# Optimization experiments

Hardware: AMD Instinct MI355X
Metric: run time of the kernel (lower is better)

The kernel has to match this reference:

```python
import jax, jax.numpy as jnp
import numpy as np
import math

D_MODEL = 96
D_STATE = 16
IMG = 32
KSZ = 3
V_LIST = [(0, 0), (0, 1), (0, -1), (1, 0), (-1, 0)]
NUM_V = len(V_LIST)
GROUPS = 4
BATCH = 4


def group_norm(x, gamma, beta, groups=GROUPS, eps=1e-5):
    B, C, H, W = x.shape
    xg = x.reshape(B, groups, C // groups, H, W)
    mu = xg.mean(axis=(2, 3, 4), keepdims=True)
    var = xg.var(axis=(2, 3, 4), keepdims=True)
    xn = ((xg - mu) * jax.lax.rsqrt(var + eps)).reshape(B, C, H, W)
    return xn * gamma[None, :, None, None] + beta[None, :, None, None]


def circ_conv(x, w, b=None):
    # circular padding then VALID conv == padding_mode='circular'
    p = w.shape[-1] // 2
    xp = jnp.pad(x, ((0, 0), (0, 0), (p, p), (p, p)), mode='wrap')
    y = jax.lax.conv_general_dilated(xp, w, (1, 1), 'VALID',
                                     dimension_numbers=('NCHW', 'OIHW', 'NCHW'))
    if b is not None:
        y = y + b[None, :, None, None]
    return y


def setup_inputs() -> dict:
    key = jax.random.key(0)
    ks = jax.random.split(key, 8)
    fan = D_MODEL * KSZ * KSZ
    inp = {
        'u_t': jax.random.normal(ks[0], (BATCH, D_MODEL, IMG, IMG), jnp.float32),
        's_prev': jax.random.normal(ks[1], (BATCH, NUM_V, D_MODEL, D_STATE, IMG, IMG), jnp.float32) * 0.1,
        'gamma': jnp.ones((D_MODEL,), jnp.float32),
        'beta': jnp.zeros((D_MODEL,), jnp.float32),
        'w_delta': jax.random.normal(ks[2], (D_MODEL, D_MODEL, KSZ, KSZ), jnp.float32) / np.sqrt(fan),
        'b_delta': jnp.zeros((D_MODEL,), jnp.float32),
        'w_B': jax.random.normal(ks[3], (D_STATE, D_MODEL, KSZ, KSZ), jnp.float32) / np.sqrt(fan),
        'w_C': jax.random.normal(ks[4], (D_STATE, D_MODEL, KSZ, KSZ), jnp.float32) / np.sqrt(fan),
        'log_A_real': jnp.full((D_MODEL, D_STATE), math.log(0.5), jnp.float32),
        'D_param': jnp.ones((D_MODEL,), jnp.float32),
        'dt_inv_softplus': jnp.asarray(math.log(math.exp(1.0) - 1.0), jnp.float32),
    }
    return inp


def reference(u_t, s_prev, gamma, beta, w_delta, b_delta, w_B, w_C, log_A_real, D_param, dt_inv_softplus):
    B, D, H, W = u_t.shape
    N = D_STATE
    u_norm = group_norm(u_t, gamma, beta)
    delta = jax.nn.softplus(circ_conv(u_norm, w_delta, b_delta) + dt_inv_softplus)
    delta = jnp.clip(delta, 1e-4, 5.0)                          # (B,D,H,W)
    B_val = circ_conv(u_norm, w_B)                               # (B,N,H,W)
    C_val = circ_conv(u_norm, w_C)                               # (B,N,H,W)
    A = -jnp.exp(log_A_real)                                     # (D,N)
    delta_bc = delta[:, :, None]                                 # (B,D,1,H,W)
    A_bar = jnp.exp(delta_bc * A[None, :, :, None, None])        # (B,D,N,H,W)
    B_bar = delta_bc * B_val[:, None]                            # (B,D,N,H,W)
    # flow transport: dest[y,x] = src[(y-vy)%H,(x-vx)%W] == roll by (vy,vx)
    s_tr = jnp.stack([jnp.roll(s_prev[:, i], shift=v, axis=(-2, -1))
                      for i, v in enumerate(V_LIST)], axis=1)    # (B,V,D,N,H,W)
    s_new = A_bar[:, None] * s_tr + B_bar[:, None] * u_t[:, None, :, None]
    y_state = jnp.sum(s_new * C_val[:, None, None], axis=3)      # (B,V,D,H,W)
    y_out = y_state + u_t[:, None] * D_param[None, None, :, None, None]
    return (y_out, s_new)
```

## Files before the change

### kernel.cpp

```cpp
#include <hip/hip_runtime.h>
#include <math.h>

#define D_MODEL 96
#define D_STATE 16
#define IMG 32
#define NUM_V 5
#define GROUPS 4
#define BATCH 4
#define HW (IMG*IMG)
#define CPG (D_MODEL/GROUPS)
#define NCOEF (D_MODEL + 2*D_STATE)
#define Y_SIZE (BATCH*NUM_V*D_MODEL*HW)

typedef float f32x4 __attribute__((ext_vector_type(4)));

__device__ __forceinline__ void nt_store4(const float4& v, float4* p) {
    f32x4 tmp = {v.x, v.y, v.z, v.w};
    __builtin_nontemporal_store(tmp, (f32x4*)p);
}

__global__ __launch_bounds__(256) void gn_kernel(const float4* __restrict__ u4,
                                                 const float* __restrict__ gamma,
                                                 const float* __restrict__ beta,
                                                 float4* __restrict__ unorm4) {
    int b = blockIdx.x >> 2, g = blockIdx.x & 3;
    int t = threadIdx.x;
    const int base4 = ((b * D_MODEL + g * CPG) * HW) >> 2;
    const int n4 = (CPG * HW) >> 2;
    float s = 0.f, s2 = 0.f;
    for (int k = t; k < n4; k += 256) {
        float4 v = u4[base4 + k];
        s += v.x + v.y + v.z + v.w;
        s2 = fmaf(v.x, v.x, fmaf(v.y, v.y, fmaf(v.z, v.z, fmaf(v.w, v.w, s2))));
    }
    for (int off = 32; off; off >>= 1) {
        s  += __shfl_down(s,  off);
        s2 += __shfl_down(s2, off);
    }
    __shared__ float red[8];
    int wid = t >> 6;
    if ((t & 63) == 0) { red[wid * 2] = s; red[wid * 2 + 1] = s2; }
    __syncthreads();
    if (t == 0) {
        float S = 0.f, S2 = 0.f;
        for (int i = 0; i < 4; ++i) { S += red[i * 2]; S2 += red[i * 2 + 1]; }
        float nf = (float)(CPG * HW);
        float mu  = S / nf;
        float var = S2 / nf - mu * mu;
        red[0] = mu;
        red[1] = rsqrtf(var + 1e-5f);
    }
    __syncthreads();
    float mu = red[0], rs = red[1];
    for (int k = t; k < n4; k += 256) {
        int c = g * CPG + (k >> 8);
        float ga = gamma[c] * rs, be = beta[c] - mu * gamma[c] * rs;
        float4 v = u4[base4 + k];
        float4 o;
        o.x = fmaf(v.x, ga, be); o.y = fmaf(v.y, ga, be);
        o.z = fmaf(v.z, ga, be); o.w = fmaf(v.w, ga, be);
        unorm4[base4 + k] = o;
    }
}

__global__ __launch_bounds__(256) void conv_kernel(const float4* __restrict__ unorm4,
                                                   const float* __restrict__ w_delta,
                                                   const float* __restrict__ b_delta,
                                                   const float* __restrict__ w_B,
                                                   const float* __restrict__ w_C,
                                                   const float* __restrict__ dt_ptr,
                                                   float4* __restrict__ coef4) {
    int bid = blockIdx.x;
    int b  = bid >> 7;
    int oc = bid & 127;
    int t  = threadIdx.x;
    int h  = t >> 3;
    int j  = t & 7;
    int lane = t & 63;
    int ll = (lane & 56) | ((j + 7) & 7);
    int rl = (lane & 56) | ((j + 1) & 7);

    const float* wp;
    float bias;
    bool is_delta = false;
    if (oc < D_MODEL) {
        wp = w_delta + oc * D_MODEL * 9;
        bias = b_delta[oc] + dt_ptr[0];
        is_delta = true;
    } else if (oc < D_MODEL + D_STATE) {
        wp = w_B + (oc - D_MODEL) * D_MODEL * 9;
        bias = 0.f;
    } else {
        wp = w_C + (oc - D_MODEL - D_STATE) * D_MODEL * 9;
        bias = 0.f;
    }
    const float4* ub4 = unorm4 + ((b * D_MODEL * HW) >> 2);

    float4 acc = {bias, bias, bias, bias};
    int hm = (h + 31) & 31, hp = (h + 1) & 31;
    int ro[3] = {hm * 8 + j, h * 8 + j, hp * 8 + j};

    for (int ic = 0; ic < D_MODEL; ++ic) {
        const float* wr = wp + ic * 9;
        const int icb = ic * 256;
        #pragma unroll
        for (int kh = 0; kh < 3; ++kh) {
            float4 q = ub4[icb + ro[kh]];
            float lw = __shfl(q.w, ll);
            float rx = __shfl(q.x, rl);
            float wa = wr[kh * 3 + 0], wb = wr[kh * 3 + 1], wc = wr[kh * 3 + 2];
            acc.x = fmaf(wa, lw,  fmaf(wb, q.x, fmaf(wc, q.y, acc.x)));
            acc.y = fmaf(wa, q.x, fmaf(wb, q.y, fmaf(wc, q.z, acc.y)));
            acc.z = fmaf(wa, q.y, fmaf(wb, q.z, fmaf(wc, q.w, acc.z)));
            acc.w = fmaf(wa, q.z, fmaf(wb, q.w, fmaf(wc, rx,  acc.w)));
        }
    }
    if (is_delta) {
        float* a = (float*)&acc;
        #pragma unroll
        for (int k = 0; k < 4; ++k) {
            float x = a[k];
            float sp = x > 20.f ? x : log1pf(__expf(x));
            a[k] = fminf(fmaxf(sp, 1e-4f), 5.f);
        }
    }
    coef4[((b * NCOEF + oc) * HW >> 2) + h * 8 + j] = acc;
}

__global__ __launch_bounds__(128) void state_kernel(const float4* __restrict__ u4,
                                                    const float4* __restrict__ s_prev4,
                                                    const float4* __restrict__ coef4,
                                                    const float* __restrict__ log_A,
                                                    const float* __restrict__ D_param,
                                                    float4* __restrict__ out4) {
    int bid = blockIdx.x;
    int b = bid / 192;
    int r = bid - b * 192;
    int d = r >> 1;
    int half = r & 1;
    int t = threadIdx.x;
    int h = half * 16 + (t >> 3);
    int j = t & 7;
    int lane = t & 63;
    int ll = (lane & 56) | ((j + 7) & 7);
    int rl = (lane & 56) | ((j + 1) & 7);
    int hw4 = h * 8 + j;

    float4 delta = coef4[((b * NCOEF + d) * HW >> 2) + hw4];
    float4 u     = u4[((b * D_MODEL + d) * HW >> 2) + hw4];
    float Dp     = D_param[d];
    const float* lA = log_A + d * D_STATE;

    int pb[NUM_V];
    #pragma unroll
    for (int i = 0; i < NUM_V; ++i)
        pb[i] = ((b * NUM_V + i) * D_MODEL + d) * (D_STATE * HW / 4);
    int hm4 = (((h + 31) & 31) * 8) + j;
    int hp4 = (((h + 1) & 31) * 8) + j;

    float4* outs4 = out4 + (Y_SIZE >> 2);

    float4 y0 = {0,0,0,0}, y1 = {0,0,0,0}, y2 = {0,0,0,0}, y3 = {0,0,0,0}, y4v = {0,0,0,0};

    #pragma unroll 2
    for (int n = 0; n < D_STATE; ++n) {
        int n4 = n * (HW / 4);
        float4 Bv = coef4[((b * NCOEF + D_MODEL + n) * HW >> 2) + hw4];
        float4 Cv = coef4[((b * NCOEF + D_MODEL + D_STATE + n) * HW >> 2) + hw4];
        float A = -__expf(lA[n]);
        float4 Ab, bu;
        Ab.x = __expf(delta.x * A); Ab.y = __expf(delta.y * A);
        Ab.z = __expf(delta.z * A); Ab.w = __expf(delta.w * A);
        bu.x = delta.x * Bv.x * u.x; bu.y = delta.y * Bv.y * u.y;
        bu.z = delta.z * Bv.z * u.z; bu.w = delta.w * Bv.w * u.w;

        {
            float4 s = s_prev4[pb[0] + n4 + hw4];
            float4 sn;
            sn.x = fmaf(Ab.x, s.x, bu.x); sn.y = fmaf(Ab.y, s.y, bu.y);
            sn.z = fmaf(Ab.z, s.z, bu.z); sn.w = fmaf(Ab.w, s.w, bu.w);
            nt_store4(sn, &outs4[pb[0] + n4 + hw4]);
            y0.x = fmaf(sn.x, Cv.x, y0.x); y0.y = fmaf(sn.y, Cv.y, y0.y);
            y0.z = fmaf(sn.z, Cv.z, y0.z); y0.w = fmaf(sn.w, Cv.w, y0.w);
        }
        {
            float4 q = s_prev4[pb[1] + n4 + hw4];
            float lw = __shfl(q.w, ll);
            float4 s = {lw, q.x, q.y, q.z};
            float4 sn;
            sn.x = fmaf(Ab.x, s.x, bu.x); sn.y = fmaf(Ab.y, s.y, bu.y);
            sn.z = fmaf(Ab.z, s.z, bu.z); sn.w = fmaf(Ab.w, s.w, bu.w);
            nt_store4(sn, &outs4[pb[1] + n4 + hw4]);
            y1.x = fmaf(sn.x, Cv.x, y1.x); y1.y = fmaf(sn.y, Cv.y, y1.y);
            y1.z = fmaf(sn.z, Cv.z, y1.z); y1.w = fmaf(sn.w, Cv.w, y1.w);
        }
        {
            float4 q = s_prev4[pb[2] + n4 + hw4];
            float rx = __shfl(q.x, rl);
            float4 s = {q.y, q.z, q.w, rx};
            float4 sn;
            sn.x = fmaf(Ab.x, s.x, bu.x); sn.y = fmaf(Ab.y, s.y, bu.y);
            sn.z = fmaf(Ab.z, s.z, bu.z); sn.w = fmaf(Ab.w, s.w, bu.w);
            nt_store4(sn, &outs4[pb[2] + n4 + hw4]);
            y2.x = fmaf(sn.x, Cv.x, y2.x); y2.y = fmaf(sn.y, Cv.y, y2.y);
            y2.z = fmaf(sn.z, Cv.z, y2.z); y2.w = fmaf(sn.w, Cv.w, y2.w);
        }
        {
            float4 s = s_prev4[pb[3] + n4 + hm4];
            float4 sn;
            sn.x = fmaf(Ab.x, s.x, bu.x); sn.y = fmaf(Ab.y, s.y, bu.y);
            sn.z = fmaf(Ab.z, s.z, bu.z); sn.w = fmaf(Ab.w, s.w, bu.w);
            nt_store4(sn, &outs4[pb[3] + n4 + hw4]);
            y3.x = fmaf(sn.x, Cv.x, y3.x); y3.y = fmaf(sn.y, Cv.y, y3.y);
            y3.z = fmaf(sn.z, Cv.z, y3.z); y3.w = fmaf(sn.w, Cv.w, y3.w);
        }
        {
            float4 s = s_prev4[pb[4] + n4 + hp4];
            float4 sn;
            sn.x = fmaf(Ab.x, s.x, bu.x); sn.y = fmaf(Ab.y, s.y, bu.y);
            sn.z = fmaf(Ab.z, s.z, bu.z); sn.w = fmaf(Ab.w, s.w, bu.w);
            nt_store4(sn, &outs4[pb[4] + n4 + hw4]);
            y4v.x = fmaf(sn.x, Cv.x, y4v.x); y4v.y = fmaf(sn.y, Cv.y, y4v.y);
            y4v.z = fmaf(sn.z, Cv.z, y4v.z); y4v.w = fmaf(sn.w, Cv.w, y4v.w);
        }
    }

    float4 du;
    du.x = u.x * Dp; du.y = u.y * Dp; du.z = u.z * Dp; du.w = u.w * Dp;
    float4* yy[NUM_V] = {&y0, &y1, &y2, &y3, &y4v};
    #pragma unroll
    for (int i = 0; i < NUM_V; ++i) {
        float4 o;
        o.x = yy[i]->x + du.x; o.y = yy[i]->y + du.y;
        o.z = yy[i]->z + du.z; o.w = yy[i]->w + du.w;
        out4[(((b * NUM_V + i) * D_MODEL + d) * HW >> 2) + hw4] = o;
    }
}

extern "C" void kernel_launch(void* const* d_in, const int* in_sizes, int n_in,
                              void* d_out, int out_size, void* d_ws, size_t ws_size,
                              hipStream_t stream) {
    const float* u_t     = (const float*)d_in[0];
    const float* s_prev  = (const float*)d_in[1];
    const float* gamma   = (const float*)d_in[2];
    const float* beta    = (const float*)d_in[3];
    const float* w_delta = (const float*)d_in[4];
    const float* b_delta = (const float*)d_in[5];
    const float* w_B     = (const float*)d_in[6];
    const float* w_C     = (const float*)d_in[7];
    const float* log_A   = (const float*)d_in[8];
    const float* D_param = (const float*)d_in[9];
    const float* dt_ptr  = (const float*)d_in[10];
    float* out = (float*)d_out;

    float* unorm = (float*)d_ws;
    float* coef  = unorm + BATCH * D_MODEL * HW;

    hipLaunchKernelGGL(gn_kernel, dim3(BATCH * GROUPS), dim3(256), 0, stream,
                       (const float4*)u_t, gamma, beta, (float4*)unorm);
    hipLaunchKernelGGL(conv_kernel, dim3(BATCH * NCOEF), dim3(256), 0, stream,
                       (const float4*)unorm, w_delta, b_delta, w_B, w_C, dt_ptr,
                       (float4*)coef);
    hipLaunchKernelGGL(state_kernel, dim3(768), dim3(128), 0, stream,
                       (const float4*)u_t, (const float4*)s_prev, (const float4*)coef,
                       log_A, D_param, (float4*)out);
}
```

Baseline: 310.2 us.

## Split state kernel across directions: one block per (batch, direction, channel)

The state kernel now launches one 256-thread block per (batch, direction, channel), each covering a full 32x32 image, instead of 128-thread blocks that each handled half an image for all five directions. Each thread processes a single direction, so it keeps one accumulator and issues one s_prev load per state step, which cuts register pressure and gives many more blocks to fill the GPU. The cost is that A_bar, B*u*delta, B and C are now recomputed and reloaded five times, once per direction.

```diff
diff --git a/kernel.cpp b/kernel.cpp
--- a/kernel.cpp
+++ b/kernel.cpp
@@ -127,46 +127,50 @@
     coef4[((b * NCOEF + oc) * HW >> 2) + h * 8 + j] = acc;
 }
 
-__global__ __launch_bounds__(128) void state_kernel(const float4* __restrict__ u4,
+__global__ __launch_bounds__(256) void state_kernel(const float4* __restrict__ u4,
                                                     const float4* __restrict__ s_prev4,
                                                     const float4* __restrict__ coef4,
                                                     const float* __restrict__ log_A,
                                                     const float* __restrict__ D_param,
                                                     float4* __restrict__ out4) {
     int bid = blockIdx.x;
-    int b = bid / 192;
-    int r = bid - b * 192;
-    int d = r >> 1;
-    int half = r & 1;
+    int b = bid / (NUM_V * D_MODEL);
+    int r = bid - b * (NUM_V * D_MODEL);
+    int i = r / D_MODEL;
+    int d = r - i * D_MODEL;
+
     int t = threadIdx.x;
-    int h = half * 16 + (t >> 3);
+    int h = t >> 3;
     int j = t & 7;
     int lane = t & 63;
     int ll = (lane & 56) | ((j + 7) & 7);
     int rl = (lane & 56) | ((j + 1) & 7);
-    int hw4 = h * 8 + j;
+    int hw4 = t;
+
+    int src4 = hw4;
+    if (i == 3) src4 = (((h + 31) & 31) << 3) | j;
+    if (i == 4) src4 = (((h + 1) & 31) << 3) | j;
+    const int mode = (i == 1) ? 1 : (i == 2) ? 2 : 0;
 
     float4 delta = coef4[((b * NCOEF + d) * HW >> 2) + hw4];
     float4 u     = u4[((b * D_MODEL + d) * HW >> 2) + hw4];
     float Dp     = D_param[d];
     const float* lA = log_A + d * D_STATE;
 
-    int pb[NUM_V];
-    #pragma unroll
-    for (int i = 0; i < NUM_V; ++i)
-        pb[i] = ((b * NUM_V + i) * D_MODEL + d) * (D_STATE * HW / 4);
-    int hm4 = (((h + 31) & 31) * 8) + j;
-    int hp4 = (((h + 1) & 31) * 8) + j;
-
-    float4* outs4 = out4 + (Y_SIZE >> 2);
-
-    float4 y0 = {0,0,0,0}, y1 = {0,0,0,0}, y2 = {0,0,0,0}, y3 = {0,0,0,0}, y4v = {0,0,0,0};
-
-    #pragma unroll 2
+    const long pb = (long)((b * NUM_V + i) * D_MODEL + d) * (D_STATE * HW / 4);
+    const float4* sp = s_prev4 + pb;
+    float4* outs = out4 + (Y_SIZE >> 2) + pb;
+    const float4* Bp = coef4 + ((b * NCOEF + D_MODEL) * HW >> 2) + hw4;
+    const float4* Cp = coef4 + ((b * NCOEF + D_MODEL + D_STATE) * HW >> 2) + hw4;
+
+    float4 y = {0.f, 0.f, 0.f, 0.f};
+
+    #pragma unroll 4
     for (int n = 0; n < D_STATE; ++n) {
         int n4 = n * (HW / 4);
-        float4 Bv = coef4[((b * NCOEF + D_MODEL + n) * HW >> 2) + hw4];
-        float4 Cv = coef4[((b * NCOEF + D_MODEL + D_STATE + n) * HW >> 2) + hw4];
+        float4 Bv = Bp[n4];
+        float4 Cv = Cp[n4];
+        float4 q  = sp[n4 + src4];
         float A = -__expf(lA[n]);
         float4 Ab, bu;
         Ab.x = __expf(delta.x * A); Ab.y = __expf(delta.y * A);
@@ -174,67 +178,27 @@
         bu.x = delta.x * Bv.x * u.x; bu.y = delta.y * Bv.y * u.y;
         bu.z = delta.z * Bv.z * u.z; bu.w = delta.w * Bv.w * u.w;
 
-        {
-            float4 s = s_prev4[pb[0] + n4 + hw4];
-            float4 sn;
-            sn.x = fmaf(Ab.x, s.x, bu.x); sn.y = fmaf(Ab.y, s.y, bu.y);
-            sn.z = fmaf(Ab.z, s.z, bu.z); sn.w = fmaf(Ab.w, s.w, bu.w);
-            nt_store4(sn, &outs4[pb[0] + n4 + hw4]);
-            y0.x = fmaf(sn.x, Cv.x, y0.x); y0.y = fmaf(sn.y, Cv.y, y0.y);
-            y0.z = fmaf(sn.z, Cv.z, y0.z); y0.w = fmaf(sn.w, Cv.w, y0.w);
+        float4 s = q;
+        if (mode == 1) {
+            float lw = __shfl(q.w, ll);
+            s.x = lw; s.y = q.x; s.z = q.y; s.w = q.z;
+        } else if (mode == 2) {
+            float rx = __shfl(q.x, rl);
+            s.x = q.y; s.y = q.z; s.z = q.w; s.w = rx;
         }
-        {
-            float4 q = s_prev4[pb[1] + n4 + hw4];
-            float lw = __shfl(q.w, ll);
-            float4 s = {lw, q.x, q.y, q.z};
-            float4 sn;
-            sn.x = fmaf(Ab.x, s.x, bu.x); sn.y = fmaf(Ab.y, s.y, bu.y);
-            sn.z = fmaf(Ab.z, s.z, bu.z); sn.w = fmaf(Ab.w, s.w, bu.w);
-            nt_store4(sn, &outs4[pb[1] + n4 + hw4]);
-            y1.x = fmaf(sn.x, Cv.x, y1.x); y1.y = fmaf(sn.y, Cv.y, y1.y);
-            y1.z = fmaf(sn.z, Cv.z, y1.z); y1.w = fmaf(sn.w, Cv.w, y1.w);
-        }
-        {
-            float4 q = s_prev4[pb[2] + n4 + hw4];
-            float rx = __shfl(q.x, rl);
-            float4 s = {q.y, q.z, q.w, rx};
-            float4 sn;
-            sn.x = fmaf(Ab.x, s.x, bu.x); sn.y = fmaf(Ab.y, s.y, bu.y);
-            sn.z = fmaf(Ab.z, s.z, bu.z); sn.w = fmaf(Ab.w, s.w, bu.w);
-            nt_store4(sn, &outs4[pb[2] + n4 + hw4]);
-            y2.x = fmaf(sn.x, Cv.x, y2.x); y2.y = fmaf(sn.y, Cv.y, y2.y);
-            y2.z = fmaf(sn.z, Cv.z, y2.z); y2.w = fmaf(sn.w, Cv.w, y2.w);
-        }
-        {
-            float4 s = s_prev4[pb[3] + n4 + hm4];
-            float4 sn;
-            sn.x = fmaf(Ab.x, s.x, bu.x); sn.y = fmaf(Ab.y, s.y, bu.y);
-            sn.z = fmaf(Ab.z, s.z, bu.z); sn.w = fmaf(Ab.w, s.w, bu.w);
-            nt_store4(sn, &outs4[pb[3] + n4 + hw4]);
-            y3.x = fmaf(sn.x, Cv.x, y3.x); y3.y = fmaf(sn.y, Cv.y, y3.y);
-            y3.z = fmaf(sn.z, Cv.z, y3.z); y3.w = fmaf(sn.w, Cv.w, y3.w);
-        }
-        {
-            float4 s = s_prev4[pb[4] + n4 + hp4];
-            float4 sn;
-            sn.x = fmaf(Ab.x, s.x, bu.x); sn.y = fmaf(Ab.y, s.y, bu.y);
-            sn.z = fmaf(Ab.z, s.z, bu.z); sn.w = fmaf(Ab.w, s.w, bu.w);
-            nt_store4(sn, &outs4[pb[4] + n4 + hw4]);
-            y4v.x = fmaf(sn.x, Cv.x, y4v.x); y4v.y = fmaf(sn.y, Cv.y, y4v.y);
-            y4v.z = fmaf(sn.z, Cv.z, y4v.z); y4v.w = fmaf(sn.w, Cv.w, y4v.w);
-        }
-    }
-
-    float4 du;
-    du.x = u.x * Dp; du.y = u.y * Dp; du.z = u.z * Dp; du.w = u.w * Dp;
-    float4* yy[NUM_V] = {&y0, &y1, &y2, &y3, &y4v};
-    #pragma unroll
-    for (int i = 0; i < NUM_V; ++i) {
-        float4 o;
-        o.x = yy[i]->x + du.x; o.y = yy[i]->y + du.y;
-        o.z = yy[i]->z + du.z; o.w = yy[i]->w + du.w;
-        out4[(((b * NUM_V + i) * D_MODEL + d) * HW >> 2) + hw4] = o;
-    }
+
+        float4 sn;
+        sn.x = fmaf(Ab.x, s.x, bu.x); sn.y = fmaf(Ab.y, s.y, bu.y);
+        sn.z = fmaf(Ab.z, s.z, bu.z); sn.w = fmaf(Ab.w, s.w, bu.w);
+        nt_store4(sn, &outs[n4 + hw4]);
+        y.x = fmaf(sn.x, Cv.x, y.x); y.y = fmaf(sn.y, Cv.y, y.y);
+        y.z = fmaf(sn.z, Cv.z, y.z); y.w = fmaf(sn.w, Cv.w, y.w);
+    }
+
+    float4 o;
+    o.x = fmaf(u.x, Dp, y.x); o.y = fmaf(u.y, Dp, y.y);
+    o.z = fmaf(u.z, Dp, y.z); o.w = fmaf(u.w, Dp, y.w);
+    out4[(((b * NUM_V + i) * D_MODEL + d) * HW >> 2) + hw4] = o;
 }
 
 extern "C" void kernel_launch(void* const* d_in, const int* in_sizes, int n_in,
@@ -261,7 +225,7 @@
     hipLaunchKernelGGL(conv_kernel, dim3(BATCH * NCOEF), dim3(256), 0, stream,
                        (const float4*)unorm, w_delta, b_delta, w_B, w_C, dt_ptr,
                        (float4*)coef);
-    hipLaunchKernelGGL(state_kernel, dim3(768), dim3(128), 0, stream,
+    hipLaunchKernelGGL(state_kernel, dim3(BATCH * NUM_V * D_MODEL), dim3(256), 0, stream,
                        (const float4*)u_t, (const float4*)s_prev, (const float4*)coef,
                        log_A, D_param, (float4*)out);
 }
```

Result: no change. 316.3 us (+2.0%).
